# Optimization experiments

Measured on AMD Instinct MI355X. Metric: run time of the kernel, lower is better.

The kernel has to match this reference:

```python
import jax, jax.numpy as jnp
import numpy as np

D_IN, D_OUT, D_K = 512, 512, 64
GAMMA = 1.0
LN_EPS = 1e-6
NEG_BIG = -1e9


def setup_inputs() -> dict:
    key = jax.random.key(0)
    ks = jax.random.split(key, 8)
    B, N = 4, 2048
    q = jax.random.normal(ks[0], (B, N, D_IN), dtype=jnp.float32)
    k = jax.random.normal(ks[1], (B, N, D_IN), dtype=jnp.float32)
    v = jax.random.normal(ks[2], (B, N, D_IN), dtype=jnp.float32)
    mask = jax.random.randint(ks[3], (B, N, N), 0, 2, dtype=jnp.int32)
    # Parameters (Linear weights stored as [in, out]; torch Linear has no bias here)
    w_qs = jax.random.normal(ks[4], (D_IN, D_K), dtype=jnp.float32) / np.sqrt(D_IN)
    w_ks = jax.random.normal(ks[5], (D_IN, D_K), dtype=jnp.float32) / np.sqrt(D_IN)
    w_fc = jax.random.normal(ks[6], (D_IN, D_OUT), dtype=jnp.float32) / np.sqrt(D_IN)
    ln_g = jnp.ones((D_OUT,), dtype=jnp.float32)
    ln_b = jnp.zeros((D_OUT,), dtype=jnp.float32)
    return {"q": q, "k": k, "v": v, "mask": mask,
            "w_qs": w_qs, "w_ks": w_ks, "w_fc": w_fc,
            "ln_g": ln_g, "ln_b": ln_b}


def _layer_norm(x, g, b):
    mu = jnp.mean(x, axis=-1, keepdims=True)
    var = jnp.mean(jnp.square(x - mu), axis=-1, keepdims=True)
    return (x - mu) * jax.lax.rsqrt(var + LN_EPS) * g + b


def reference(q, k, v, mask, w_qs, w_ks, w_fc, ln_g, ln_b):
    scale = D_K ** 0.5
    qp = jnp.einsum('bnd,dk->bnk', q, w_qs)            # [B,N,d_k]
    kp = jnp.einsum('bnd,dk->bnk', k, w_ks)            # [B,N,d_k]
    scores = jnp.einsum('bik,bjk->bij', qp / scale, kp)  # [B,N,N]
    scores = jnp.where(mask == 0, jnp.float32(NEG_BIG), scores)
    attn = jax.nn.softmax(scores, axis=-1) * GAMMA      # [B,N,N]
    out = jnp.einsum('bij,bjd->bid', attn, v) + v       # attn@V + V residual
    out = jnp.einsum('bnd,de->bne', out, w_fc)          # fc (dropout = identity in eval)
    out = _layer_norm(out, ln_g, ln_b)
    return (out, attn)
```

## Files before the change

### kernel.cpp

```cpp
#include <hip/hip_runtime.h>
#include <hip/hip_bf16.h>

#define BB  4
#define SEQ 2048
#define DIM 512
#define DK  64

typedef __attribute__((ext_vector_type(8))) short short8;
typedef __attribute__((ext_vector_type(4))) float f32x4;

__device__ __forceinline__ unsigned int pack_bf2(float a, float b){
  __hip_bfloat16 ha = __float2bfloat16(a), hb = __float2bfloat16(b);
  unsigned short ua = __builtin_bit_cast(unsigned short, ha);
  unsigned short ub = __builtin_bit_cast(unsigned short, hb);
  return (unsigned int)ua | ((unsigned int)ub << 16);
}
__device__ __forceinline__ unsigned short to_bf(float a){
  return __builtin_bit_cast(unsigned short, __float2bfloat16(a));
}

template<bool BTRANS, bool MASKED, bool RESID, int NGRP>
__global__ __launch_bounds__(256) void gemm_kernel(
    const float* __restrict__ A, const float* __restrict__ Bm, float* __restrict__ C,
    const float* __restrict__ resid, const int* __restrict__ mask,
    int K, int lda, int ldb, int ldc,
    long sA, long sB, long sC, long sR, long sM, float scale)
{
  constexpr int TM = 128, TK = 32, TN = 64*NGRP;
  __shared__ float As[TK][TM+4];
  __shared__ float Bs[TK][TN+4];
  const int z = blockIdx.z;
  A += z*sA; Bm += z*sB; C += z*sC;
  const float* rp = nullptr; const int* mp = nullptr;
  if constexpr (RESID)  rp = resid + z*sR;
  if constexpr (MASKED) mp = mask  + z*sM;
  const int m0 = blockIdx.x*TM, n0 = blockIdx.y*TN;
  const int tid = threadIdx.x, tx = tid & 15, ty = tid >> 4;
  float acc[2][NGRP][4][4] = {};

  for (int k0 = 0; k0 < K; k0 += TK) {
    #pragma unroll
    for (int e = tid; e < TM*TK/4; e += 256) {
      int m = e >> 3, k4 = (e & 7) << 2;
      float4 a = *(const float4*)&A[(long)(m0+m)*lda + k0 + k4];
      As[k4+0][m] = a.x; As[k4+1][m] = a.y; As[k4+2][m] = a.z; As[k4+3][m] = a.w;
    }
    if constexpr (BTRANS) {
      #pragma unroll
      for (int e = tid; e < TN*TK/4; e += 256) {
        int n = e >> 3, k4 = (e & 7) << 2;
        float4 b = *(const float4*)&Bm[(long)(n0+n)*ldb + k0 + k4];
        Bs[k4+0][n] = b.x; Bs[k4+1][n] = b.y; Bs[k4+2][n] = b.z; Bs[k4+3][n] = b.w;
      }
    } else {
      constexpr int TN4 = TN/4;
      #pragma unroll
      for (int e = tid; e < TK*TN4; e += 256) {
        int kk = e / TN4, n4 = (e % TN4) << 2;
        *(float4*)&Bs[kk][n4] = *(const float4*)&Bm[(long)(k0+kk)*ldb + n0 + n4];
      }
    }
    __syncthreads();
    #pragma unroll
    for (int kk = 0; kk < TK; kk++) {
      float av[2][4];
      float bv[NGRP][4];
      *(float4*)av[0] = *(const float4*)&As[kk][ty*4];
      *(float4*)av[1] = *(const float4*)&As[kk][64 + ty*4];
      #pragma unroll
      for (int g = 0; g < NGRP; g++)
        *(float4*)bv[g] = *(const float4*)&Bs[kk][g*64 + tx*4];
      #pragma unroll
      for (int mg = 0; mg < 2; mg++)
        #pragma unroll
        for (int r = 0; r < 4; r++)
          #pragma unroll
          for (int g = 0; g < NGRP; g++)
            #pragma unroll
            for (int c = 0; c < 4; c++)
              acc[mg][g][r][c] = fmaf(av[mg][r], bv[g][c], acc[mg][g][r][c]);
    }
    __syncthreads();
  }

  #pragma unroll
  for (int mg = 0; mg < 2; mg++) {
    #pragma unroll
    for (int r = 0; r < 4; r++) {
      const int m = m0 + mg*64 + ty*4 + r;
      #pragma unroll
      for (int g = 0; g < NGRP; g++) {
        const int n = n0 + g*64 + tx*4;
        float4 v;
        v.x = acc[mg][g][r][0]*scale; v.y = acc[mg][g][r][1]*scale;
        v.z = acc[mg][g][r][2]*scale; v.w = acc[mg][g][r][3]*scale;
        if constexpr (RESID) {
          float4 rv = *(const float4*)&rp[(long)m*ldc + n];
          v.x += rv.x; v.y += rv.y; v.z += rv.z; v.w += rv.w;
        }
        if constexpr (MASKED) {
          int4 mv = *(const int4*)&mp[(long)m*ldc + n];
          if (!mv.x) v.x = -1e9f;
          if (!mv.y) v.y = -1e9f;
          if (!mv.z) v.z = -1e9f;
          if (!mv.w) v.w = -1e9f;
        }
        *(float4*)&C[(long)m*ldc + n] = v;
      }
    }
  }
}

__global__ __launch_bounds__(256) void proj_mfma_kernel(
    const float* __restrict__ q, const float* __restrict__ k,
    const float* __restrict__ w_qs, const float* __restrict__ w_ks,
    unsigned short* __restrict__ qp, unsigned short* __restrict__ kp)
{
  __shared__ unsigned short As[64][72];
  __shared__ unsigned short Bs[64][72];
  const int z = blockIdx.y;
  const float* A = z ? k : q;
  const float* W = z ? w_ks : w_qs;
  unsigned short* D = z ? kp : qp;
  const float scale = z ? 1.0f : 0.125f;
  const long m0 = (long)blockIdx.x * 64;
  const int tid = threadIdx.x;
  const int lane = tid & 63, wid = tid >> 6;
  const int qq = lane >> 4, l16 = lane & 15;
  f32x4 acc[4] = {};

  for (int k0 = 0; k0 < DIM; k0 += 64) {
    {
      int r = tid >> 2, h = tid & 3;
      const float* src = &A[(m0+r)*DIM + k0 + h*16];
      float4 x0 = *(const float4*)src,     x1 = *(const float4*)(src+4),
             x2 = *(const float4*)(src+8), x3 = *(const float4*)(src+12);
      unsigned int tmp[8] = {pack_bf2(x0.x,x0.y),pack_bf2(x0.z,x0.w),
                             pack_bf2(x1.x,x1.y),pack_bf2(x1.z,x1.w),
                             pack_bf2(x2.x,x2.y),pack_bf2(x2.z,x2.w),
                             pack_bf2(x3.x,x3.y),pack_bf2(x3.z,x3.w)};
      *(uint4*)&As[r][h*16]   = ((uint4*)tmp)[0];
      *(uint4*)&As[r][h*16+8] = ((uint4*)tmp)[1];
    }
    {
      int kk = tid >> 2, n4 = (tid & 3) * 16;
      const float* src = &W[(long)(k0+kk)*DK + n4];
      float4 y0 = *(const float4*)src,     y1 = *(const float4*)(src+4),
             y2 = *(const float4*)(src+8), y3 = *(const float4*)(src+12);
      float yv[16] = {y0.x,y0.y,y0.z,y0.w, y1.x,y1.y,y1.z,y1.w,
                      y2.x,y2.y,y2.z,y2.w, y3.x,y3.y,y3.z,y3.w};
      #pragma unroll
      for (int j = 0; j < 16; j++)
        Bs[n4+j][kk] = to_bf(yv[j]);
    }
    __syncthreads();
    #pragma unroll
    for (int ks = 0; ks < 2; ks++) {
      short8 af = *(const short8*)&As[wid*16 + l16][ks*32 + qq*8];
      #pragma unroll
      for (int nt = 0; nt < 4; nt++) {
        short8 bf = *(const short8*)&Bs[nt*16 + l16][ks*32 + qq*8];
        acc[nt] = __builtin_amdgcn_mfma_f32_16x16x32_bf16(af, bf, acc[nt], 0, 0, 0);
      }
    }
    __syncthreads();
  }

  #pragma unroll
  for (int nt = 0; nt < 4; nt++) {
    const int col = nt*16 + l16;
    #pragma unroll
    for (int r = 0; r < 4; r++) {
      const long row = m0 + wid*16 + qq*4 + r;
      D[row*DK + col] = to_bf(acc[nt][r] * scale);
    }
  }
}

__global__ __launch_bounds__(256) void scores_mfma_kernel(
    const unsigned short* __restrict__ qp, const unsigned short* __restrict__ kp,
    const int* __restrict__ mask, float* __restrict__ scores)
{
  __shared__ unsigned short As[128][72];
  __shared__ unsigned short Bs[128][72];
  const int b = blockIdx.z;
  const unsigned short* ap = qp + (long)b*SEQ*DK;
  const unsigned short* bp = kp + (long)b*SEQ*DK;
  const int* mp = mask + (long)b*SEQ*SEQ;
  float* sp = scores + (long)b*SEQ*SEQ;
  const int m0 = blockIdx.x*128, n0 = blockIdx.y*128;
  const int tid = threadIdx.x;
  const int lane = tid & 63, wid = tid >> 6;
  const int wr = wid >> 1, wc = wid & 1;
  const int qq = lane >> 4, l16 = lane & 15;

  {
    int r = tid >> 1, h = tid & 1;
    const uint4* srcA = (const uint4*)&ap[(long)(m0+r)*DK + h*32];
    const uint4* srcB = (const uint4*)&bp[(long)(n0+r)*DK + h*32];
    uint4 a0=srcA[0],a1=srcA[1],a2=srcA[2],a3=srcA[3];
    uint4 b0=srcB[0],b1=srcB[1],b2=srcB[2],b3=srcB[3];
    *(uint4*)&As[r][h*32+ 0]=a0; *(uint4*)&As[r][h*32+ 8]=a1;
    *(uint4*)&As[r][h*32+16]=a2; *(uint4*)&As[r][h*32+24]=a3;
    *(uint4*)&Bs[r][h*32+ 0]=b0; *(uint4*)&Bs[r][h*32+ 8]=b1;
    *(uint4*)&Bs[r][h*32+16]=b2; *(uint4*)&Bs[r][h*32+24]=b3;
  }
  __syncthreads();

  f32x4 acc[4][4] = {};
  #pragma unroll
  for (int ks = 0; ks < 2; ks++) {
    short8 af[4], bf[4];
    #pragma unroll
    for (int mt = 0; mt < 4; mt++)
      af[mt] = *(const short8*)&As[wr*64 + mt*16 + l16][ks*32 + qq*8];
    #pragma unroll
    for (int nt = 0; nt < 4; nt++)
      bf[nt] = *(const short8*)&Bs[wc*64 + nt*16 + l16][ks*32 + qq*8];
    #pragma unroll
    for (int mt = 0; mt < 4; mt++)
      #pragma unroll
      for (int nt = 0; nt < 4; nt++)
        acc[mt][nt] = __builtin_amdgcn_mfma_f32_16x16x32_bf16(af[mt], bf[nt], acc[mt][nt], 0, 0, 0);
  }

  #pragma unroll
  for (int mt = 0; mt < 4; mt++) {
    #pragma unroll
    for (int nt = 0; nt < 4; nt++) {
      const int col = n0 + wc*64 + nt*16 + l16;
      #pragma unroll
      for (int r = 0; r < 4; r++) {
        const long row = m0 + wr*64 + mt*16 + qq*4 + r;
        float vv = acc[mt][nt][r];
        if (mp[row*SEQ + col] == 0) vv = -1e9f;
        sp[row*SEQ + col] = vv;
      }
    }
  }
}

__global__ __launch_bounds__(256) void softmax_kernel(float* __restrict__ attn)
{
  const long row = blockIdx.x;
  float* p = attn + row*SEQ;
  const int t = threadIdx.x;
  float4 a = ((const float4*)p)[t];
  float4 b = ((const float4*)p)[t + 256];
  float f[8] = {a.x,a.y,a.z,a.w,b.x,b.y,b.z,b.w};
  float M = f[0];
  #pragma unroll
  for (int i = 1; i < 8; i++) M = fmaxf(M, f[i]);
  #pragma unroll
  for (int o = 1; o < 64; o <<= 1) M = fmaxf(M, __shfl_xor(M, o));
  __shared__ float r1[4], r2[4];
  if ((t & 63) == 0) r1[t >> 6] = M;
  __syncthreads();
  M = fmaxf(fmaxf(r1[0], r1[1]), fmaxf(r1[2], r1[3]));
  float s = 0.f;
  #pragma unroll
  for (int i = 0; i < 8; i++) { f[i] = __expf(f[i] - M); s += f[i]; }
  #pragma unroll
  for (int o = 1; o < 64; o <<= 1) s += __shfl_xor(s, o);
  if ((t & 63) == 0) r2[t >> 6] = s;
  __syncthreads();
  s = (r2[0] + r2[1]) + (r2[2] + r2[3]);
  const float inv = 1.0f / s;
  a.x = f[0]*inv; a.y = f[1]*inv; a.z = f[2]*inv; a.w = f[3]*inv;
  b.x = f[4]*inv; b.y = f[5]*inv; b.z = f[6]*inv; b.w = f[7]*inv;
  ((float4*)p)[t] = a;
  ((float4*)p)[t + 256] = b;
}

__global__ __launch_bounds__(256) void fc_ln_kernel(
    float* __restrict__ X, const float* __restrict__ W,
    const float* __restrict__ g, const float* __restrict__ b)
{
  __shared__ float As[32][32+4];
  __shared__ float Bs[32][512+4];
  const int tid = threadIdx.x;
  const long r0 = (long)blockIdx.x * 32;
  const int tx = tid & 63, ty = tid >> 6;
  float acc[8][8] = {};

  for (int k0 = 0; k0 < DIM; k0 += 32) {
    {
      int m = tid >> 3, k4 = (tid & 7) << 2;
      float4 a = *(const float4*)&X[(r0+m)*DIM + k0 + k4];
      As[k4+0][m] = a.x; As[k4+1][m] = a.y; As[k4+2][m] = a.z; As[k4+3][m] = a.w;
    }
    #pragma unroll
    for (int e = tid; e < 32*128; e += 256) {
      int kk = e >> 7, n4 = (e & 127) << 2;
      *(float4*)&Bs[kk][n4] = *(const float4*)&W[(long)(k0+kk)*DIM + n4];
    }
    __syncthreads();
    #pragma unroll
    for (int kk = 0; kk < 32; kk++) {
      float a[8], bb[8];
      *(float4*)&a[0]  = *(const float4*)&As[kk][ty*8];
      *(float4*)&a[4]  = *(const float4*)&As[kk][ty*8+4];
      *(float4*)&bb[0] = *(const float4*)&Bs[kk][tx*8];
      *(float4*)&bb[4] = *(const float4*)&Bs[kk][tx*8+4];
      #pragma unroll
      for (int r = 0; r < 8; r++)
        #pragma unroll
        for (int c = 0; c < 8; c++)
          acc[r][c] = fmaf(a[r], bb[c], acc[r][c]);
    }
    __syncthreads();
  }

  float gv[8], bv[8];
  *(float4*)&gv[0] = *(const float4*)&g[tx*8];
  *(float4*)&gv[4] = *(const float4*)&g[tx*8+4];
  *(float4*)&bv[0] = *(const float4*)&b[tx*8];
  *(float4*)&bv[4] = *(const float4*)&b[tx*8+4];

  #pragma unroll
  for (int r = 0; r < 8; r++) {
    float s = 0.f, sq = 0.f;
    #pragma unroll
    for (int c = 0; c < 8; c++) { s += acc[r][c]; sq += acc[r][c]*acc[r][c]; }
    #pragma unroll
    for (int o = 1; o < 64; o <<= 1) { s += __shfl_xor(s, o); sq += __shfl_xor(sq, o); }
    const float mean = s * (1.0f/DIM);
    float var = sq * (1.0f/DIM) - mean*mean;
    var = fmaxf(var, 0.0f);
    const float rs = rsqrtf(var + 1e-6f);
    float o0[8];
    #pragma unroll
    for (int c = 0; c < 8; c++) o0[c] = (acc[r][c] - mean)*rs*gv[c] + bv[c];
    float* dst = &X[(r0 + ty*8 + r)*DIM + tx*8];
    *(float4*)&dst[0] = *(const float4*)&o0[0];
    *(float4*)&dst[4] = *(const float4*)&o0[4];
  }
}

__global__ __launch_bounds__(256) void transpose_v_kernel(
    const float* __restrict__ v, unsigned short* __restrict__ vT)
{
  __shared__ float T[64][65];
  const int b = blockIdx.z;
  const int k0 = blockIdx.x*64, n0 = blockIdx.y*64;
  const float* vb = v + (long)b*SEQ*DIM;
  unsigned short* tb = vT + (long)b*DIM*SEQ;
  const int t = threadIdx.x;
  {
    int kk = t >> 2, nq = (t & 3)*16;
    const float4* src = (const float4*)&vb[(long)(k0+kk)*DIM + n0 + nq];
    #pragma unroll
    for (int j = 0; j < 4; j++) {
      float4 x = src[j];
      T[kk][nq+4*j+0] = x.x; T[kk][nq+4*j+1] = x.y;
      T[kk][nq+4*j+2] = x.z; T[kk][nq+4*j+3] = x.w;
    }
  }
  __syncthreads();
  {
    int n = t >> 2, kq = (t & 3)*16;
    unsigned int w[8];
    #pragma unroll
    for (int j = 0; j < 8; j++)
      w[j] = pack_bf2(T[kq+2*j][n], T[kq+2*j+1][n]);
    unsigned short* dst = &tb[(long)(n0+n)*SEQ + k0 + kq];
    *(uint4*)&dst[0] = *(uint4*)&w[0];
    *(uint4*)&dst[8] = *(uint4*)&w[4];
  }
}

__global__ __launch_bounds__(256) void transpose_w_kernel(
    const float* __restrict__ w, unsigned short* __restrict__ wT)
{
  __shared__ float T[64][65];
  const int k0 = blockIdx.x*64, n0 = blockIdx.y*64;
  const int t = threadIdx.x;
  {
    int kk = t >> 2, nq = (t & 3)*16;
    const float4* src = (const float4*)&w[(long)(k0+kk)*DIM + n0 + nq];
    #pragma unroll
    for (int j = 0; j < 4; j++) {
      float4 x = src[j];
      T[kk][nq+4*j+0] = x.x; T[kk][nq+4*j+1] = x.y;
      T[kk][nq+4*j+2] = x.z; T[kk][nq+4*j+3] = x.w;
    }
  }
  __syncthreads();
  {
    int n = t >> 2, kq = (t & 3)*16;
    unsigned int wv[8];
    #pragma unroll
    for (int j = 0; j < 8; j++)
      wv[j] = pack_bf2(T[kq+2*j][n], T[kq+2*j+1][n]);
    unsigned short* dst = &wT[(long)(n0+n)*DIM + k0 + kq];
    *(uint4*)&dst[0] = *(uint4*)&wv[0];
    *(uint4*)&dst[8] = *(uint4*)&wv[4];
  }
}

__global__ __launch_bounds__(256) void attn_v_mfma_kernel(
    const float* __restrict__ attn, const unsigned short* __restrict__ vT,
    const float* __restrict__ v, float* __restrict__ out)
{
  __shared__ unsigned short As[128][72];
  __shared__ unsigned short Bs[128][72];
  const int b = blockIdx.z;
  const float* ap = attn + (long)b*SEQ*SEQ;
  const unsigned short* bp = vT + (long)b*DIM*SEQ;
  const float* vp = v + (long)b*SEQ*DIM;
  float* op = out + (long)b*SEQ*DIM;
  const int m0 = blockIdx.x*128, n0 = blockIdx.y*128;
  const int tid = threadIdx.x;
  const int lane = tid & 63, wid = tid >> 6;
  const int wr = wid >> 1, wc = wid & 1;
  const int q = lane >> 4, l16 = lane & 15;

  f32x4 acc[4][4] = {};

  for (int k0 = 0; k0 < SEQ; k0 += 64) {
    {
      int r = tid >> 1, h = tid & 1;
      const float4* src = (const float4*)&ap[(long)(m0+r)*SEQ + k0 + h*32];
      unsigned int tmp[16];
      #pragma unroll
      for (int j = 0; j < 8; j++) {
        float4 x = src[j];
        tmp[2*j]   = pack_bf2(x.x, x.y);
        tmp[2*j+1] = pack_bf2(x.z, x.w);
      }
      #pragma unroll
      for (int j = 0; j < 4; j++)
        *(uint4*)&As[r][h*32 + 8*j] = ((const uint4*)tmp)[j];
    }
    {
      int n = tid >> 1, h = tid & 1;
      const uint4* src = (const uint4*)&bp[(long)(n0+n)*SEQ + k0 + h*32];
      uint4 b0 = src[0], b1 = src[1], b2 = src[2], b3 = src[3];
      *(uint4*)&Bs[n][h*32 +  0] = b0;
      *(uint4*)&Bs[n][h*32 +  8] = b1;
      *(uint4*)&Bs[n][h*32 + 16] = b2;
      *(uint4*)&Bs[n][h*32 + 24] = b3;
    }
    __syncthreads();
    #pragma unroll
    for (int ks = 0; ks < 2; ks++) {
      short8 af[4], bf[4];
      #pragma unroll
      for (int mt = 0; mt < 4; mt++)
        af[mt] = *(const short8*)&As[wr*64 + mt*16 + l16][ks*32 + q*8];
      #pragma unroll
      for (int nt = 0; nt < 4; nt++)
        bf[nt] = *(const short8*)&Bs[wc*64 + nt*16 + l16][ks*32 + q*8];
      #pragma unroll
      for (int mt = 0; mt < 4; mt++)
        #pragma unroll
        for (int nt = 0; nt < 4; nt++)
          acc[mt][nt] = __builtin_amdgcn_mfma_f32_16x16x32_bf16(af[mt], bf[nt], acc[mt][nt], 0, 0, 0);
    }
    __syncthreads();
  }

  #pragma unroll
  for (int mt = 0; mt < 4; mt++) {
    #pragma unroll
    for (int nt = 0; nt < 4; nt++) {
      const int col = n0 + wc*64 + nt*16 + l16;
      #pragma unroll
      for (int r = 0; r < 4; r++) {
        const int row = m0 + wr*64 + mt*16 + q*4 + r;
        op[(long)row*DIM + col] = acc[mt][nt][r] + vp[(long)row*DIM + col];
      }
    }
  }
}

__global__ __launch_bounds__(256) void fc_ln_mfma_kernel(
    float* __restrict__ X, const unsigned short* __restrict__ wT,
    const float* __restrict__ g, const float* __restrict__ b)
{
  __shared__ unsigned short As[32][72];
  __shared__ unsigned short Bs[512][72];
  __shared__ float red_s[4][32], red_q[4][32];
  __shared__ float gs[512], bs[512];
  const int tid = threadIdx.x;
  const long r0 = (long)blockIdx.x * 32;
  const int lane = tid & 63, wid = tid >> 6;
  const int q = lane >> 4, l16 = lane & 15;

  gs[tid] = g[tid]; gs[tid+256] = g[tid+256];
  bs[tid] = b[tid]; bs[tid+256] = b[tid+256];

  f32x4 acc[2][8] = {};

  for (int k0 = 0; k0 < DIM; k0 += 64) {
    {
      int r = tid >> 3, h = tid & 7;
      const float* src = &X[(r0+r)*DIM + k0 + h*8];
      float4 x0 = *(const float4*)src, x1 = *(const float4*)(src+4);
      unsigned int tmp[4] = {pack_bf2(x0.x,x0.y), pack_bf2(x0.z,x0.w),
                             pack_bf2(x1.x,x1.y), pack_bf2(x1.z,x1.w)};
      *(uint4*)&As[r][h*8] = *(uint4*)tmp;
    }
    #pragma unroll
    for (int e = tid; e < 4096; e += 256) {
      int n = e >> 3, j = e & 7;
      *(uint4*)&Bs[n][j*8] = *(const uint4*)&wT[(long)n*DIM + k0 + j*8];
    }
    __syncthreads();
    #pragma unroll
    for (int ks = 0; ks < 2; ks++) {
      short8 af[2], bf[8];
      #pragma unroll
      for (int mt = 0; mt < 2; mt++)
        af[mt] = *(const short8*)&As[mt*16 + l16][ks*32 + q*8];
      #pragma unroll
      for (int nt = 0; nt < 8; nt++)
        bf[nt] = *(const short8*)&Bs[wid*128 + nt*16 + l16][ks*32 + q*8];
      #pragma unroll
      for (int mt = 0; mt < 2; mt++)
        #pragma unroll
        for (int nt = 0; nt < 8; nt++)
          acc[mt][nt] = __builtin_amdgcn_mfma_f32_16x16x32_bf16(af[mt], bf[nt], acc[mt][nt], 0, 0, 0);
    }
    __syncthreads();
  }

  #pragma unroll
  for (int mt = 0; mt < 2; mt++) {
    #pragma unroll
    for (int r = 0; r < 4; r++) {
      float s = 0.f, z = 0.f;
      #pragma unroll
      for (int nt = 0; nt < 8; nt++) { float v = acc[mt][nt][r]; s += v; z += v*v; }
      #pragma unroll
      for (int o = 1; o < 16; o <<= 1) { s += __shfl_xor(s, o); z += __shfl_xor(z, o); }
      if (l16 == 0) { red_s[wid][mt*16 + q*4 + r] = s; red_q[wid][mt*16 + q*4 + r] = z; }
    }
  }
  __syncthreads();

  float mean[2][4], rstd[2][4];
  #pragma unroll
  for (int mt = 0; mt < 2; mt++)
    #pragma unroll
    for (int r = 0; r < 4; r++) {
      const int row = mt*16 + q*4 + r;
      float s = (red_s[0][row] + red_s[1][row]) + (red_s[2][row] + red_s[3][row]);
      float z = (red_q[0][row] + red_q[1][row]) + (red_q[2][row] + red_q[3][row]);
      float mu = s * (1.0f/DIM);
      float var = z * (1.0f/DIM) - mu*mu;
      var = fmaxf(var, 0.0f);
      mean[mt][r] = mu;
      rstd[mt][r] = rsqrtf(var + 1e-6f);
    }

  #pragma unroll
  for (int mt = 0; mt < 2; mt++) {
    #pragma unroll
    for (int nt = 0; nt < 8; nt++) {
      const int col = wid*128 + nt*16 + l16;
      const float gg = gs[col], bb = bs[col];
      #pragma unroll
      for (int r = 0; r < 4; r++) {
        const long row = r0 + mt*16 + q*4 + r;
        X[row*DIM + col] = (acc[mt][nt][r] - mean[mt][r])*rstd[mt][r]*gg + bb;
      }
    }
  }
}

extern "C" void kernel_launch(void* const* d_in, const int* in_sizes, int n_in,
                              void* d_out, int out_size, void* d_ws, size_t ws_size,
                              hipStream_t stream) {
  const float* q    = (const float*)d_in[0];
  const float* k    = (const float*)d_in[1];
  const float* v    = (const float*)d_in[2];
  const int*   mask = (const int*)d_in[3];
  const float* w_qs = (const float*)d_in[4];
  const float* w_ks = (const float*)d_in[5];
  const float* w_fc = (const float*)d_in[6];
  const float* ln_g = (const float*)d_in[7];
  const float* ln_b = (const float*)d_in[8];

  float* out   = (float*)d_out;
  float* attnF = out + (long)BB*SEQ*DIM;

  unsigned short* qp = (unsigned short*)out;
  unsigned short* kp = qp + (long)BB*SEQ*DK;

  const long NN2 = (long)SEQ*SEQ;
  const long ND  = (long)SEQ*DIM;

  const size_t vT_bytes = (size_t)BB*DIM*SEQ*sizeof(unsigned short);
  const size_t wT_bytes = (size_t)DIM*DIM*sizeof(unsigned short);
  const bool fast  = (ws_size >= vT_bytes);
  const bool fast2 = (ws_size >= vT_bytes + wT_bytes);

  proj_mfma_kernel<<<dim3(BB*SEQ/64, 2, 1), 256, 0, stream>>>(q, k, w_qs, w_ks, qp, kp);
  scores_mfma_kernel<<<dim3(SEQ/128, SEQ/128, BB), 256, 0, stream>>>(qp, kp, mask, attnF);
  softmax_kernel<<<dim3(BB*SEQ,1,1), 256, 0, stream>>>(attnF);
  if (fast) {
    unsigned short* vT = (unsigned short*)d_ws;
    transpose_v_kernel<<<dim3(SEQ/64, DIM/64, BB), 256, 0, stream>>>(v, vT);
    attn_v_mfma_kernel<<<dim3(SEQ/128, DIM/128, BB), 256, 0, stream>>>(attnF, vT, v, out);
  } else {
    gemm_kernel<false,false,true,2><<<dim3(SEQ/128,DIM/128,BB), 256, 0, stream>>>(
        attnF, v, out, v, nullptr, SEQ, SEQ, DIM, DIM, NN2, ND, ND, ND, 0, 1.0f);
  }
  if (fast2) {
    unsigned short* wT = (unsigned short*)d_ws + (size_t)BB*DIM*SEQ;
    transpose_w_kernel<<<dim3(DIM/64, DIM/64, 1), 256, 0, stream>>>(w_fc, wT);
    fc_ln_mfma_kernel<<<dim3(BB*SEQ/32,1,1), 256, 0, stream>>>(out, wT, ln_g, ln_b);
  } else {
    fc_ln_kernel<<<dim3(BB*SEQ/32,1,1), 256, 0, stream>>>(out, w_fc, ln_g, ln_b);
  }
}
```

Before: 348.4 us.

## Fuse mask into softmax and feed bf16 attention copy to attn@V

The mask load and select move from the scores epilogue into the softmax kernel, so the scores kernel only writes. Softmax also writes a bf16 copy of the probabilities to workspace. A new attn@V kernel reads that bf16 copy with 128x64 tiles, which halves the attention read traffic and removes the in-kernel fp32-to-bf16 conversion. The cost is an extra 32 MB bf16 write and a larger workspace requirement; if the workspace is too small, the code falls back to the old path.

```diff
diff --git a/kernel.cpp b/kernel.cpp
--- a/kernel.cpp
+++ b/kernel.cpp
@@ -179,14 +179,13 @@
 
 __global__ __launch_bounds__(256) void scores_mfma_kernel(
     const unsigned short* __restrict__ qp, const unsigned short* __restrict__ kp,
-    const int* __restrict__ mask, float* __restrict__ scores)
+    float* __restrict__ scores)
 {
   __shared__ unsigned short As[128][72];
   __shared__ unsigned short Bs[128][72];
   const int b = blockIdx.z;
   const unsigned short* ap = qp + (long)b*SEQ*DK;
   const unsigned short* bp = kp + (long)b*SEQ*DK;
-  const int* mp = mask + (long)b*SEQ*SEQ;
   float* sp = scores + (long)b*SEQ*SEQ;
   const int m0 = blockIdx.x*128, n0 = blockIdx.y*128;
   const int tid = threadIdx.x;
@@ -232,22 +231,33 @@
       #pragma unroll
       for (int r = 0; r < 4; r++) {
         const long row = m0 + wr*64 + mt*16 + qq*4 + r;
-        float vv = acc[mt][nt][r];
-        if (mp[row*SEQ + col] == 0) vv = -1e9f;
-        sp[row*SEQ + col] = vv;
-      }
-    }
-  }
-}
-
-__global__ __launch_bounds__(256) void softmax_kernel(float* __restrict__ attn)
+        sp[row*SEQ + col] = acc[mt][nt][r];
+      }
+    }
+  }
+}
+
+__global__ __launch_bounds__(256) void softmax_kernel2(
+    float* __restrict__ attn, const int* __restrict__ mask,
+    unsigned short* __restrict__ attnB)
 {
   const long row = blockIdx.x;
   float* p = attn + row*SEQ;
+  const int* mp = mask + row*SEQ;
   const int t = threadIdx.x;
   float4 a = ((const float4*)p)[t];
   float4 b = ((const float4*)p)[t + 256];
+  int4 ma = ((const int4*)mp)[t];
+  int4 mb = ((const int4*)mp)[t + 256];
   float f[8] = {a.x,a.y,a.z,a.w,b.x,b.y,b.z,b.w};
+  if (!ma.x) f[0] = -1e9f;
+  if (!ma.y) f[1] = -1e9f;
+  if (!ma.z) f[2] = -1e9f;
+  if (!ma.w) f[3] = -1e9f;
+  if (!mb.x) f[4] = -1e9f;
+  if (!mb.y) f[5] = -1e9f;
+  if (!mb.z) f[6] = -1e9f;
+  if (!mb.w) f[7] = -1e9f;
   float M = f[0];
   #pragma unroll
   for (int i = 1; i < 8; i++) M = fmaxf(M, f[i]);
@@ -266,135 +276,86 @@
   __syncthreads();
   s = (r2[0] + r2[1]) + (r2[2] + r2[3]);
   const float inv = 1.0f / s;
-  a.x = f[0]*inv; a.y = f[1]*inv; a.z = f[2]*inv; a.w = f[3]*inv;
-  b.x = f[4]*inv; b.y = f[5]*inv; b.z = f[6]*inv; b.w = f[7]*inv;
+  #pragma unroll
+  for (int i = 0; i < 8; i++) f[i] *= inv;
+  a.x = f[0]; a.y = f[1]; a.z = f[2]; a.w = f[3];
+  b.x = f[4]; b.y = f[5]; b.z = f[6]; b.w = f[7];
   ((float4*)p)[t] = a;
   ((float4*)p)[t + 256] = b;
-}
-
-__global__ __launch_bounds__(256) void fc_ln_kernel(
-    float* __restrict__ X, const float* __restrict__ W,
-    const float* __restrict__ g, const float* __restrict__ b)
-{
-  __shared__ float As[32][32+4];
-  __shared__ float Bs[32][512+4];
+  if (attnB) {
+    unsigned short* pb = attnB + row*SEQ;
+    uint2 w0 = { pack_bf2(f[0], f[1]), pack_bf2(f[2], f[3]) };
+    uint2 w1 = { pack_bf2(f[4], f[5]), pack_bf2(f[6], f[7]) };
+    *(uint2*)&pb[t*4]        = w0;
+    *(uint2*)&pb[1024 + t*4] = w1;
+  }
+}
+
+__global__ __launch_bounds__(256) void attn_v_mfma2_kernel(
+    const unsigned short* __restrict__ attnB, const unsigned short* __restrict__ vT,
+    const float* __restrict__ v, float* __restrict__ out)
+{
+  __shared__ unsigned short As[128][72];
+  __shared__ unsigned short Bs[64][72];
+  const int b = blockIdx.z;
+  const unsigned short* ap = attnB + (long)b*SEQ*SEQ;
+  const unsigned short* bp = vT + (long)b*DIM*SEQ;
+  const float* vp = v + (long)b*SEQ*DIM;
+  float* op = out + (long)b*SEQ*DIM;
+  const int m0 = blockIdx.x*128, n0 = blockIdx.y*64;
   const int tid = threadIdx.x;
-  const long r0 = (long)blockIdx.x * 32;
-  const int tx = tid & 63, ty = tid >> 6;
-  float acc[8][8] = {};
-
-  for (int k0 = 0; k0 < DIM; k0 += 32) {
+  const int lane = tid & 63, wid = tid >> 6;
+  const int q = lane >> 4, l16 = lane & 15;
+
+  f32x4 acc[2][4] = {};
+
+  for (int k0 = 0; k0 < SEQ; k0 += 64) {
     {
-      int m = tid >> 3, k4 = (tid & 7) << 2;
-      float4 a = *(const float4*)&X[(r0+m)*DIM + k0 + k4];
-      As[k4+0][m] = a.x; As[k4+1][m] = a.y; As[k4+2][m] = a.z; As[k4+3][m] = a.w;
-    }
-    #pragma unroll
-    for (int e = tid; e < 32*128; e += 256) {
-      int kk = e >> 7, n4 = (e & 127) << 2;
-      *(float4*)&Bs[kk][n4] = *(const float4*)&W[(long)(k0+kk)*DIM + n4];
-    }
-    __syncthreads();
-    #pragma unroll
-    for (int kk = 0; kk < 32; kk++) {
-      float a[8], bb[8];
-      *(float4*)&a[0]  = *(const float4*)&As[kk][ty*8];
-      *(float4*)&a[4]  = *(const float4*)&As[kk][ty*8+4];
-      *(float4*)&bb[0] = *(const float4*)&Bs[kk][tx*8];
-      *(float4*)&bb[4] = *(const float4*)&Bs[kk][tx*8+4];
-      #pragma unroll
-      for (int r = 0; r < 8; r++)
+      int r = tid >> 1, h = tid & 1;
+      const uint4* src = (const uint4*)&ap[(long)(m0+r)*SEQ + k0 + h*32];
+      uint4 a0 = src[0], a1 = src[1], a2 = src[2], a3 = src[3];
+      *(uint4*)&As[r][h*32 +  0] = a0;
+      *(uint4*)&As[r][h*32 +  8] = a1;
+      *(uint4*)&As[r][h*32 + 16] = a2;
+      *(uint4*)&As[r][h*32 + 24] = a3;
+    }
+    {
+      int n = tid >> 2, h = tid & 3;
+      const uint4* src = (const uint4*)&bp[(long)(n0+n)*SEQ + k0 + h*16];
+      uint4 b0 = src[0], b1 = src[1];
+      *(uint4*)&Bs[n][h*16 + 0] = b0;
+      *(uint4*)&Bs[n][h*16 + 8] = b1;
+    }
+    __syncthreads();
+    #pragma unroll
+    for (int ks = 0; ks < 2; ks++) {
+      short8 af[2], bf[4];
+      #pragma unroll
+      for (int mt = 0; mt < 2; mt++)
+        af[mt] = *(const short8*)&As[wid*32 + mt*16 + l16][ks*32 + q*8];
+      #pragma unroll
+      for (int nt = 0; nt < 4; nt++)
+        bf[nt] = *(const short8*)&Bs[nt*16 + l16][ks*32 + q*8];
+      #pragma unroll
+      for (int mt = 0; mt < 2; mt++)
         #pragma unroll
-        for (int c = 0; c < 8; c++)
-          acc[r][c] = fmaf(a[r], bb[c], acc[r][c]);
-    }
-    __syncthreads();
-  }
-
-  float gv[8], bv[8];
-  *(float4*)&gv[0] = *(const float4*)&g[tx*8];
-  *(float4*)&gv[4] = *(const float4*)&g[tx*8+4];
-  *(float4*)&bv[0] = *(const float4*)&b[tx*8];
-  *(float4*)&bv[4] = *(const float4*)&b[tx*8+4];
-
-  #pragma unroll
-  for (int r = 0; r < 8; r++) {
-    float s = 0.f, sq = 0.f;
-    #pragma unroll
-    for (int c = 0; c < 8; c++) { s += acc[r][c]; sq += acc[r][c]*acc[r][c]; }
-    #pragma unroll
-    for (int o = 1; o < 64; o <<= 1) { s += __shfl_xor(s, o); sq += __shfl_xor(sq, o); }
-    const float mean = s * (1.0f/DIM);
-    float var = sq * (1.0f/DIM) - mean*mean;
-    var = fmaxf(var, 0.0f);
-    const float rs = rsqrtf(var + 1e-6f);
-    float o0[8];
-    #pragma unroll
-    for (int c = 0; c < 8; c++) o0[c] = (acc[r][c] - mean)*rs*gv[c] + bv[c];
-    float* dst = &X[(r0 + ty*8 + r)*DIM + tx*8];
-    *(float4*)&dst[0] = *(const float4*)&o0[0];
-    *(float4*)&dst[4] = *(const float4*)&o0[4];
-  }
-}
-
-__global__ __launch_bounds__(256) void transpose_v_kernel(
-    const float* __restrict__ v, unsigned short* __restrict__ vT)
-{
-  __shared__ float T[64][65];
-  const int b = blockIdx.z;
-  const int k0 = blockIdx.x*64, n0 = blockIdx.y*64;
-  const float* vb = v + (long)b*SEQ*DIM;
-  unsigned short* tb = vT + (long)b*DIM*SEQ;
-  const int t = threadIdx.x;
-  {
-    int kk = t >> 2, nq = (t & 3)*16;
-    const float4* src = (const float4*)&vb[(long)(k0+kk)*DIM + n0 + nq];
-    #pragma unroll
-    for (int j = 0; j < 4; j++) {
-      float4 x = src[j];
-      T[kk][nq+4*j+0] = x.x; T[kk][nq+4*j+1] = x.y;
-      T[kk][nq+4*j+2] = x.z; T[kk][nq+4*j+3] = x.w;
-    }
-  }
-  __syncthreads();
-  {
-    int n = t >> 2, kq = (t & 3)*16;
-    unsigned int w[8];
-    #pragma unroll
-    for (int j = 0; j < 8; j++)
-      w[j] = pack_bf2(T[kq+2*j][n], T[kq+2*j+1][n]);
-    unsigned short* dst = &tb[(long)(n0+n)*SEQ + k0 + kq];
-    *(uint4*)&dst[0] = *(uint4*)&w[0];
-    *(uint4*)&dst[8] = *(uint4*)&w[4];
-  }
-}
-
-__global__ __launch_bounds__(256) void transpose_w_kernel(
-    const float* __restrict__ w, unsigned short* __restrict__ wT)
-{
-  __shared__ float T[64][65];
-  const int k0 = blockIdx.x*64, n0 = blockIdx.y*64;
-  const int t = threadIdx.x;
-  {
-    int kk = t >> 2, nq = (t & 3)*16;
-    const float4* src = (const float4*)&w[(long)(k0+kk)*DIM + n0 + nq];
-    #pragma unroll
-    for (int j = 0; j < 4; j++) {
-      float4 x = src[j];
-      T[kk][nq+4*j+0] = x.x; T[kk][nq+4*j+1] = x.y;
-      T[kk][nq+4*j+2] = x.z; T[kk][nq+4*j+3] = x.w;
-    }
-  }
-  __syncthreads();
-  {
-    int n = t >> 2, kq = (t & 3)*16;
-    unsigned int wv[8];
-    #pragma unroll
-    for (int j = 0; j < 8; j++)
-      wv[j] = pack_bf2(T[kq+2*j][n], T[kq+2*j+1][n]);
-    unsigned short* dst = &wT[(long)(n0+n)*DIM + k0 + kq];
-    *(uint4*)&dst[0] = *(uint4*)&wv[0];
-    *(uint4*)&dst[8] = *(uint4*)&wv[4];
+        for (int nt = 0; nt < 4; nt++)
+          acc[mt][nt] = __builtin_amdgcn_mfma_f32_16x16x32_bf16(af[mt], bf[nt], acc[mt][nt], 0, 0, 0);
+    }
+    __syncthreads();
+  }
+
+  #pragma unroll
+  for (int mt = 0; mt < 2; mt++) {
+    #pragma unroll
+    for (int nt = 0; nt < 4; nt++) {
+      const int col = n0 + nt*16 + l16;
+      #pragma unroll
+      for (int r = 0; r < 4; r++) {
+        const int row = m0 + wid*32 + mt*16 + q*4 + r;
+        op[(long)row*DIM + col] = acc[mt][nt][r] + vp[(long)row*DIM + col];
+      }
+    }
   }
 }
 
@@ -474,6 +435,132 @@
   }
 }
 
+__global__ __launch_bounds__(256) void fc_ln_kernel(
+    float* __restrict__ X, const float* __restrict__ W,
+    const float* __restrict__ g, const float* __restrict__ b)
+{
+  __shared__ float As[32][32+4];
+  __shared__ float Bs[32][512+4];
+  const int tid = threadIdx.x;
+  const long r0 = (long)blockIdx.x * 32;
+  const int tx = tid & 63, ty = tid >> 6;
+  float acc[8][8] = {};
+
+  for (int k0 = 0; k0 < DIM; k0 += 32) {
+    {
+      int m = tid >> 3, k4 = (tid & 7) << 2;
+      float4 a = *(const float4*)&X[(r0+m)*DIM + k0 + k4];
+      As[k4+0][m] = a.x; As[k4+1][m] = a.y; As[k4+2][m] = a.z; As[k4+3][m] = a.w;
+    }
+    #pragma unroll
+    for (int e = tid; e < 32*128; e += 256) {
+      int kk = e >> 7, n4 = (e & 127) << 2;
+      *(float4*)&Bs[kk][n4] = *(const float4*)&W[(long)(k0+kk)*DIM + n4];
+    }
+    __syncthreads();
+    #pragma unroll
+    for (int kk = 0; kk < 32; kk++) {
+      float a[8], bb[8];
+      *(float4*)&a[0]  = *(const float4*)&As[kk][ty*8];
+      *(float4*)&a[4]  = *(const float4*)&As[kk][ty*8+4];
+      *(float4*)&bb[0] = *(const float4*)&Bs[kk][tx*8];
+      *(float4*)&bb[4] = *(const float4*)&Bs[kk][tx*8+4];
+      #pragma unroll
+      for (int r = 0; r < 8; r++)
+        #pragma unroll
+        for (int c = 0; c < 8; c++)
+          acc[r][c] = fmaf(a[r], bb[c], acc[r][c]);
+    }
+    __syncthreads();
+  }
+
+  float gv[8], bv[8];
+  *(float4*)&gv[0] = *(const float4*)&g[tx*8];
+  *(float4*)&gv[4] = *(const float4*)&g[tx*8+4];
+  *(float4*)&bv[0] = *(const float4*)&b[tx*8];
+  *(float4*)&bv[4] = *(const float4*)&b[tx*8+4];
+
+  #pragma unroll
+  for (int r = 0; r < 8; r++) {
+    float s = 0.f, sq = 0.f;
+    #pragma unroll
+    for (int c = 0; c < 8; c++) { s += acc[r][c]; sq += acc[r][c]*acc[r][c]; }
+    #pragma unroll
+    for (int o = 1; o < 64; o <<= 1) { s += __shfl_xor(s, o); sq += __shfl_xor(sq, o); }
+    const float mean = s * (1.0f/DIM);
+    float var = sq * (1.0f/DIM) - mean*mean;
+    var = fmaxf(var, 0.0f);
+    const float rs = rsqrtf(var + 1e-6f);
+    float o0[8];
+    #pragma unroll
+    for (int c = 0; c < 8; c++) o0[c] = (acc[r][c] - mean)*rs*gv[c] + bv[c];
+    float* dst = &X[(r0 + ty*8 + r)*DIM + tx*8];
+    *(float4*)&dst[0] = *(const float4*)&o0[0];
+    *(float4*)&dst[4] = *(const float4*)&o0[4];
+  }
+}
+
+__global__ __launch_bounds__(256) void transpose_v_kernel(
+    const float* __restrict__ v, unsigned short* __restrict__ vT)
+{
+  __shared__ float T[64][65];
+  const int b = blockIdx.z;
+  const int k0 = blockIdx.x*64, n0 = blockIdx.y*64;
+  const float* vb = v + (long)b*SEQ*DIM;
+  unsigned short* tb = vT + (long)b*DIM*SEQ;
+  const int t = threadIdx.x;
+  {
+    int kk = t >> 2, nq = (t & 3)*16;
+    const float4* src = (const float4*)&vb[(long)(k0+kk)*DIM + n0 + nq];
+    #pragma unroll
+    for (int j = 0; j < 4; j++) {
+      float4 x = src[j];
+      T[kk][nq+4*j+0] = x.x; T[kk][nq+4*j+1] = x.y;
+      T[kk][nq+4*j+2] = x.z; T[kk][nq+4*j+3] = x.w;
+    }
+  }
+  __syncthreads();
+  {
+    int n = t >> 2, kq = (t & 3)*16;
+    unsigned int w[8];
+    #pragma unroll
+    for (int j = 0; j < 8; j++)
+      w[j] = pack_bf2(T[kq+2*j][n], T[kq+2*j+1][n]);
+    unsigned short* dst = &tb[(long)(n0+n)*SEQ + k0 + kq];
+    *(uint4*)&dst[0] = *(uint4*)&w[0];
+    *(uint4*)&dst[8] = *(uint4*)&w[4];
+  }
+}
+
+__global__ __launch_bounds__(256) void transpose_w_kernel(
+    const float* __restrict__ w, unsigned short* __restrict__ wT)
+{
+  __shared__ float T[64][65];
+  const int k0 = blockIdx.x*64, n0 = blockIdx.y*64;
+  const int t = threadIdx.x;
+  {
+    int kk = t >> 2, nq = (t & 3)*16;
+    const float4* src = (const float4*)&w[(long)(k0+kk)*DIM + n0 + nq];
+    #pragma unroll
+    for (int j = 0; j < 4; j++) {
+      float4 x = src[j];
+      T[kk][nq+4*j+0] = x.x; T[kk][nq+4*j+1] = x.y;
+      T[kk][nq+4*j+2] = x.z; T[kk][nq+4*j+3] = x.w;
+    }
+  }
+  __syncthreads();
+  {
+    int n = t >> 2, kq = (t & 3)*16;
+    unsigned int wv[8];
+    #pragma unroll
+    for (int j = 0; j < 8; j++)
+      wv[j] = pack_bf2(T[kq+2*j][n], T[kq+2*j+1][n]);
+    unsigned short* dst = &wT[(long)(n0+n)*DIM + k0 + kq];
+    *(uint4*)&dst[0] = *(uint4*)&wv[0];
+    *(uint4*)&dst[8] = *(uint4*)&wv[4];
+  }
+}
+
 __global__ __launch_bounds__(256) void fc_ln_mfma_kernel(
     float* __restrict__ X, const unsigned short* __restrict__ wT,
     const float* __restrict__ g, const float* __restrict__ b)
@@ -591,24 +678,33 @@
   const long NN2 = (long)SEQ*SEQ;
   const long ND  = (long)SEQ*DIM;
 
-  const size_t vT_bytes = (size_t)BB*DIM*SEQ*sizeof(unsigned short);
-  const size_t wT_bytes = (size_t)DIM*DIM*sizeof(unsigned short);
+  const size_t vT_bytes    = (size_t)BB*DIM*SEQ*2;
+  const size_t wT_bytes    = (size_t)DIM*DIM*2;
+  const size_t attnB_bytes = (size_t)BB*SEQ*SEQ*2;
   const bool fast  = (ws_size >= vT_bytes);
   const bool fast2 = (ws_size >= vT_bytes + wT_bytes);
+  const bool fast3 = (ws_size >= vT_bytes + wT_bytes + attnB_bytes);
+
+  unsigned short* vT    = (unsigned short*)d_ws;
+  unsigned short* wT    = vT + (size_t)BB*DIM*SEQ;
+  unsigned short* attnB = wT + (size_t)DIM*DIM;
 
   proj_mfma_kernel<<<dim3(BB*SEQ/64, 2, 1), 256, 0, stream>>>(q, k, w_qs, w_ks, qp, kp);
-  scores_mfma_kernel<<<dim3(SEQ/128, SEQ/128, BB), 256, 0, stream>>>(qp, kp, mask, attnF);
-  softmax_kernel<<<dim3(BB*SEQ,1,1), 256, 0, stream>>>(attnF);
+  scores_mfma_kernel<<<dim3(SEQ/128, SEQ/128, BB), 256, 0, stream>>>(qp, kp, attnF);
+  softmax_kernel2<<<dim3(BB*SEQ,1,1), 256, 0, stream>>>(
+      attnF, mask, fast3 ? attnB : (unsigned short*)nullptr);
   if (fast) {
-    unsigned short* vT = (unsigned short*)d_ws;
     transpose_v_kernel<<<dim3(SEQ/64, DIM/64, BB), 256, 0, stream>>>(v, vT);
-    attn_v_mfma_kernel<<<dim3(SEQ/128, DIM/128, BB), 256, 0, stream>>>(attnF, vT, v, out);
+    if (fast3) {
+      attn_v_mfma2_kernel<<<dim3(SEQ/128, DIM/64, BB), 256, 0, stream>>>(attnB, vT, v, out);
+    } else {
+      attn_v_mfma_kernel<<<dim3(SEQ/128, DIM/128, BB), 256, 0, stream>>>(attnF, vT, v, out);
+    }
   } else {
     gemm_kernel<false,false,true,2><<<dim3(SEQ/128,DIM/128,BB), 256, 0, stream>>>(
         attnF, v, out, v, nullptr, SEQ, SEQ, DIM, DIM, NN2, ND, ND, ND, 0, 1.0f);
   }
   if (fast2) {
-    unsigned short* wT = (unsigned short*)d_ws + (size_t)BB*DIM*SEQ;
     transpose_w_kernel<<<dim3(DIM/64, DIM/64, 1), 256, 0, stream>>>(w_fc, wT);
     fc_ln_mfma_kernel<<<dim3(BB*SEQ/32,1,1), 256, 0, stream>>>(out, wT, ln_g, ln_b);
   } else {
```

Measured after the change: 309.0 us. -11.3%, faster.
